# Kernel tuning notes

Measured on AMD Instinct MI355X. Metric: run time of the kernel, lower is better.

Reference implementation:

```python
import jax, jax.numpy as jnp
import numpy as np
import math

H = 12  # heads (init kwarg)
KEEP_RATE = 0.7  # forward arg keep_rate (< 1 -> token pruning path)


def setup_inputs() -> dict:
    key = jax.random.key(0)
    k0, k1, k2 = jax.random.split(key, 3)
    b, n, c = 32, 577, 768  # ViT-B/16 @ 384px: 576 patches + CLS
    x = jax.random.normal(k0, (b, n, c), dtype=jnp.float32)
    # nn.Linear(dim, dim*3) and nn.Linear(dim, dim); kaiming-ish scale
    W_qkv = jax.random.normal(k1, (c, 3 * c), dtype=jnp.float32) / np.sqrt(c).astype(np.float32)
    b_qkv = jnp.zeros((3 * c,), dtype=jnp.float32)
    W_out = jax.random.normal(k2, (c, c), dtype=jnp.float32) / np.sqrt(c).astype(np.float32)
    b_out = jnp.zeros((c,), dtype=jnp.float32)
    return {"x": x, "keep_rate": KEEP_RATE, "W_qkv": W_qkv, "b_qkv": b_qkv,
            "W_out": W_out, "b_out": b_out}


def reference(x, keep_rate, W_qkv, b_qkv, W_out, b_out):
    b, n, c = x.shape
    d = c // H
    scale = (c / H) ** -0.5
    # qkv projection + split into heads: 'b n (h d) -> b h n d'
    qkv = x @ W_qkv + b_qkv                      # [b, n, 3c]
    q, k, v = jnp.split(qkv, 3, axis=-1)
    split_heads = lambda t: t.reshape(b, n, H, d).transpose(0, 2, 1, 3)
    q, k, v = split_heads(q), split_heads(k), split_heads(v)
    dots = jnp.einsum('bhid,bhjd->bhij', q, k) * scale   # [b,h,n,n]
    attention = jax.nn.softmax(dots, axis=-1)
    out = jnp.einsum('bhij,bhjd->bhid', attention, v)    # [b,h,n,d]
    out = out.transpose(0, 2, 1, 3).reshape(b, n, c)     # 'b h n d -> b n (h d)'
    out = out @ W_out + b_out                            # to_out (dropout=0)
    final_tokens = n - 1
    if keep_rate < 1:
        final_tokens = math.ceil(keep_rate * final_tokens)
        # CLS-token attention to patch tokens, averaged over heads
        class_attention = attention[:, :, 0, 1:].mean(axis=1)   # [b, n-1]
        _, ind = jax.lax.top_k(class_attention, final_tokens)    # [b, final_tokens]
        ind = jnp.sort(ind, axis=1)
        index = jnp.broadcast_to(ind[:, :, None], (b, final_tokens, c))
        return (x, index, ind, class_attention, final_tokens)
    return (out, None, None, None, final_tokens)
```

## Files before the change

### kernel.cpp

```cpp
#include <hip/hip_runtime.h>
#include <math.h>

#define BATCH 32
#define NTOK 577
#define NPATCH 576
#define CDIM 768
#define HEADS 12
#define DHEAD 64
#define W3 2304
#define FT 404

#define WS_WTIL  24576
#define WS_DBIAS 319488
#define WS_DOTS  319872
#define WS_IND   541440

#define O_X      0ULL
#define O_INDEX  14180352ULL
#define O_IND    24109056ULL
#define O_CA     24121984ULL
#define O_FT     24140416ULL

#define NIDX4  2482176
#define NCOPY4 3545088

__global__ __launch_bounds__(512) void k_fold(const float* __restrict__ x,
                                              const float* __restrict__ W,
                                              const float* __restrict__ bq,
                                              float* __restrict__ wtil,
                                              float* __restrict__ dbias) {
    __shared__ float x0s[CDIM];
    __shared__ float red[512];
    __shared__ float qs[DHEAD];
    const int b = blockIdx.x, h = blockIdx.y, tid = threadIdx.x;
    if (tid < CDIM / 4)
        ((float4*)x0s)[tid] = ((const float4*)(x + (size_t)b * NTOK * CDIM))[tid];
    __syncthreads();
    {
        const int d = tid & 63, seg = tid >> 6;
        const float* Wq = W + h * DHEAD + d;
        const int c0 = seg * 96;
        float acc = 0.f;
        #pragma unroll 32
        for (int c = c0; c < c0 + 96; c++) acc += x0s[c] * Wq[(size_t)c * W3];
        red[tid] = acc;
    }
    __syncthreads();
    if (tid < DHEAD) {
        float q = red[tid];
        #pragma unroll
        for (int s = 1; s < 8; s++) q += red[tid + s * 64];
        q += bq[h * DHEAD + tid];
        qs[tid] = q;
        float t = q * bq[CDIM + h * DHEAD + tid];
        #pragma unroll
        for (int off = 32; off; off >>= 1) t += __shfl_down(t, off);
        if (tid == 0) dbias[b * HEADS + h] = t;
    }
    __syncthreads();
    for (int c = tid; c < CDIM; c += 512) {
        const float* wr = W + (size_t)c * W3 + CDIM + h * DHEAD;
        float acc = 0.f;
        #pragma unroll
        for (int d = 0; d < DHEAD; d += 4) {
            float4 a = *reinterpret_cast<const float4*>(wr + d);
            acc += a.x * qs[d] + a.y * qs[d + 1] + a.z * qs[d + 2] + a.w * qs[d + 3];
        }
        wtil[((size_t)b * HEADS + h) * CDIM + c] = acc;
    }
}

#define LOADG(A, G)                                                               \
    {                                                                             \
        _Pragma("unroll")                                                         \
        for (int u = 0; u < 4; u++) {                                             \
            const int j = jbase + (G) * 4 + u;                                    \
            if (j < NTOK) {                                                       \
                const float4* xp =                                                \
                    (const float4*)(x + ((size_t)b * NTOK + j) * CDIM);           \
                A[u][0] = xp[lane]; A[u][1] = xp[64 + lane]; A[u][2] = xp[128 + lane]; \
            } else {                                                              \
                A[u][0] = A[u][1] = A[u][2] = make_float4(0.f, 0.f, 0.f, 0.f);    \
            }                                                                     \
        }                                                                         \
    }

#define COMPG(A, G)                                                               \
    {                                                                             \
        float acc[4][3];                                                          \
        _Pragma("unroll")                                                         \
        for (int u = 0; u < 4; u++) { acc[u][0] = acc[u][1] = acc[u][2] = 0.f; }  \
        _Pragma("unroll")                                                         \
        for (int i = 0; i < 3; i++)                                               \
            _Pragma("unroll")                                                     \
            for (int u = 0; u < 4; u++)                                           \
                _Pragma("unroll")                                                 \
                for (int hh = 0; hh < 3; hh++)                                    \
                    acc[u][hh] += A[u][i].x * wr[hh][i].x + A[u][i].y * wr[hh][i].y \
                                + A[u][i].z * wr[hh][i].z + A[u][i].w * wr[hh][i].w; \
        _Pragma("unroll")                                                         \
        for (int off = 32; off; off >>= 1)                                        \
            _Pragma("unroll")                                                     \
            for (int u = 0; u < 4; u++)                                           \
                _Pragma("unroll")                                                 \
                for (int hh = 0; hh < 3; hh++)                                    \
                    acc[u][hh] += __shfl_xor(acc[u][hh], off);                    \
        if (lane == 0) {                                                          \
            _Pragma("unroll")                                                     \
            for (int u = 0; u < 4; u++) {                                         \
                const int j = jbase + (G) * 4 + u;                                \
                if (j < NTOK) {                                                   \
                    _Pragma("unroll")                                             \
                    for (int hh = 0; hh < 3; hh++)                                \
                        dots[((size_t)b * HEADS + h0 + hh) * NTOK + j] =          \
                            0.125f * (acc[u][hh] + db[hh]);                       \
                }                                                                 \
            }                                                                     \
        }                                                                         \
    }

__global__ __launch_bounds__(256, 3) void k_dots(const float* __restrict__ x,
                                                 const float* __restrict__ wtil,
                                                 const float* __restrict__ dbias,
                                                 float* __restrict__ dots) {
    const int b = blockIdx.x, tid = threadIdx.x;
    const int w = tid >> 6, lane = tid & 63, h0 = w * 3;
    float4 wr[3][3];
    float db[3];
    #pragma unroll
    for (int hh = 0; hh < 3; hh++) {
        #pragma unroll
        for (int i = 0; i < 3; i++)
            wr[hh][i] = *reinterpret_cast<const float4*>(
                wtil + ((size_t)b * HEADS + h0 + hh) * CDIM + i * 256 + lane * 4);
        db[hh] = dbias[b * HEADS + h0 + hh];
    }
    const int jbase = blockIdx.y * 16;
    float4 abuf[4][3], nbuf[4][3];
    LOADG(abuf, 0);
    LOADG(nbuf, 1);
    COMPG(abuf, 0);
    LOADG(abuf, 2);
    COMPG(nbuf, 1);
    LOADG(nbuf, 3);
    COMPG(abuf, 2);
    COMPG(nbuf, 3);
}

__global__ __launch_bounds__(512) void k_catopk(const float* __restrict__ dots,
                                                float* __restrict__ out,
                                                int* __restrict__ indws,
                                                int write_ft) {
    __shared__ float dl[HEADS * NTOK];
    __shared__ float mh[HEADS], sh[HEADS];
    __shared__ unsigned vals[NPATCH];
    __shared__ unsigned long long segmask[9];
    __shared__ int segoff[9];
    const int b = blockIdx.x, tid = threadIdx.x;
    {
        const float4* s4 = (const float4*)(dots + (size_t)b * HEADS * NTOK);
        float4* d4 = (float4*)dl;
        for (int i = tid; i < HEADS * NTOK / 4; i += 512) d4[i] = s4[i];
    }
    __syncthreads();
    const int w = tid >> 6, lane = tid & 63;
    for (int h = w; h < HEADS; h += 8) {
        const float* row = dl + h * NTOK;
        float m = -3.4e38f;
        for (int j = lane; j < NTOK; j += 64) m = fmaxf(m, row[j]);
        #pragma unroll
        for (int off = 32; off; off >>= 1) m = fmaxf(m, __shfl_xor(m, off));
        float s = 0.f;
        for (int j = lane; j < NTOK; j += 64) s += expf(row[j] - m);
        #pragma unroll
        for (int off = 32; off; off >>= 1) s += __shfl_xor(s, off);
        if (lane == 0) { mh[h] = m; sh[h] = s; }
    }
    __syncthreads();
    for (int t = tid; t < NPATCH; t += 512) {
        float ca = 0.f;
        #pragma unroll
        for (int h = 0; h < HEADS; h++)
            ca += expf(dl[h * NTOK + 1 + t] - mh[h]) / sh[h];
        ca *= (1.f / 12.f);
        out[O_CA + (size_t)b * NPATCH + t] = ca;
        vals[t] = __float_as_uint(ca);
    }
    __syncthreads();
    {
        const uint4* v4 = (const uint4*)vals;
        for (int s = w; s < 9; s += 8) {
            const int t = s * 64 + lane;
            const unsigned myv = vals[t];
            int rank = 0;
            #pragma unroll 8
            for (int j4 = 0; j4 < NPATCH / 4; j4++) {
                const uint4 vv = v4[j4];
                const int j = j4 * 4;
                rank += (vv.x > myv) || (vv.x == myv && j     < t);
                rank += (vv.y > myv) || (vv.y == myv && j + 1 < t);
                rank += (vv.z > myv) || (vv.z == myv && j + 2 < t);
                rank += (vv.w > myv) || (vv.w == myv && j + 3 < t);
            }
            const unsigned long long mask = __ballot(rank < FT);
            if (lane == 0) segmask[s] = mask;
        }
    }
    __syncthreads();
    if (tid == 0) {
        int acc = 0;
        #pragma unroll
        for (int s = 0; s < 9; s++) { segoff[s] = acc; acc += __popcll(segmask[s]); }
    }
    __syncthreads();
    for (int s = w; s < 9; s += 8) {
        const int t = s * 64 + lane;
        const unsigned long long mask = segmask[s];
        if ((mask >> lane) & 1ull) {
            const int pos = segoff[s] + __popcll(mask & ((1ull << lane) - 1ull));
            indws[b * FT + pos] = t;
            out[O_IND + (size_t)b * FT + pos] = (float)t;
        }
    }
    if (b == 0 && tid == 0 && write_ft) out[O_FT] = (float)FT;
}

__global__ __launch_bounds__(256) void k_bcast(const int* __restrict__ ind,
                                               const float* __restrict__ x,
                                               float* __restrict__ out) {
    const float4* x4 = (const float4*)x;
    float4* o4 = (float4*)(out + O_X);
    float4* i4 = (float4*)(out + O_INDEX);
    const unsigned stride = gridDim.x * 256u;
    for (unsigned g = blockIdx.x * 256u + threadIdx.x; g < NIDX4 + NCOPY4; g += stride) {
        if (g < NCOPY4) {
            o4[g] = x4[g];
        } else {
            const unsigned e = g - NCOPY4;
            const unsigned row = e / 192u;
            const float v = (float)ind[row];
            float4 o; o.x = v; o.y = v; o.z = v; o.w = v;
            i4[e] = o;
        }
    }
}

extern "C" void kernel_launch(void* const* d_in, const int* in_sizes, int n_in,
                              void* d_out, int out_size, void* d_ws, size_t ws_size,
                              hipStream_t stream) {
    const float* x  = (const float*)d_in[0];
    const float* W  = (const float*)d_in[2];
    const float* bq = (const float*)d_in[3];
    float* ws = (float*)d_ws;
    float* out = (float*)d_out;

    k_fold<<<dim3(BATCH, HEADS), 512, 0, stream>>>(x, W, bq, ws + WS_WTIL, ws + WS_DBIAS);
    k_dots<<<dim3(BATCH, 37), 256, 0, stream>>>(x, ws + WS_WTIL, ws + WS_DBIAS,
                                                ws + WS_DOTS);
    const int write_ft = (out_size > (int)O_FT) ? 1 : 0;
    k_catopk<<<BATCH, 512, 0, stream>>>(ws + WS_DOTS, out, (int*)(ws + WS_IND), write_ft);
    k_bcast<<<2048, 256, 0, stream>>>((const int*)(ws + WS_IND), x, out);
}
```

Measured before the change: 236.5 us.

## Tile k_dots over 64 tokens with shared-memory staging of x and folded weights

Rewrites the CLS-query dot kernel so each block handles 64 tokens for all 12 heads. The block stages the folded weights and 128-column chunks of x in LDS. Each thread accumulates a 4x12 register tile, and partial sums are reduced through shuffles and a shared buffer. This cuts the grid from 37 to 10 blocks per batch and removes the per-token full-wave shuffle reductions, at the cost of about 70KB of LDS per block, which lowers occupancy, and more __syncthreads barriers.

```diff
diff --git a/kernel.cpp b/kernel.cpp
--- a/kernel.cpp
+++ b/kernel.cpp
@@ -23,6 +23,8 @@
 
 #define NIDX4  2482176
 #define NCOPY4 3545088
+
+#define XROW 132
 
 __global__ __launch_bounds__(512) void k_fold(const float* __restrict__ x,
                                               const float* __restrict__ W,
@@ -70,81 +72,87 @@
     }
 }
 
-#define LOADG(A, G)                                                               \
-    {                                                                             \
-        _Pragma("unroll")                                                         \
-        for (int u = 0; u < 4; u++) {                                             \
-            const int j = jbase + (G) * 4 + u;                                    \
-            if (j < NTOK) {                                                       \
-                const float4* xp =                                                \
-                    (const float4*)(x + ((size_t)b * NTOK + j) * CDIM);           \
-                A[u][0] = xp[lane]; A[u][1] = xp[64 + lane]; A[u][2] = xp[128 + lane]; \
-            } else {                                                              \
-                A[u][0] = A[u][1] = A[u][2] = make_float4(0.f, 0.f, 0.f, 0.f);    \
-            }                                                                     \
-        }                                                                         \
-    }
-
-#define COMPG(A, G)                                                               \
-    {                                                                             \
-        float acc[4][3];                                                          \
-        _Pragma("unroll")                                                         \
-        for (int u = 0; u < 4; u++) { acc[u][0] = acc[u][1] = acc[u][2] = 0.f; }  \
-        _Pragma("unroll")                                                         \
-        for (int i = 0; i < 3; i++)                                               \
-            _Pragma("unroll")                                                     \
-            for (int u = 0; u < 4; u++)                                           \
-                _Pragma("unroll")                                                 \
-                for (int hh = 0; hh < 3; hh++)                                    \
-                    acc[u][hh] += A[u][i].x * wr[hh][i].x + A[u][i].y * wr[hh][i].y \
-                                + A[u][i].z * wr[hh][i].z + A[u][i].w * wr[hh][i].w; \
-        _Pragma("unroll")                                                         \
-        for (int off = 32; off; off >>= 1)                                        \
-            _Pragma("unroll")                                                     \
-            for (int u = 0; u < 4; u++)                                           \
-                _Pragma("unroll")                                                 \
-                for (int hh = 0; hh < 3; hh++)                                    \
-                    acc[u][hh] += __shfl_xor(acc[u][hh], off);                    \
-        if (lane == 0) {                                                          \
-            _Pragma("unroll")                                                     \
-            for (int u = 0; u < 4; u++) {                                         \
-                const int j = jbase + (G) * 4 + u;                                \
-                if (j < NTOK) {                                                   \
-                    _Pragma("unroll")                                             \
-                    for (int hh = 0; hh < 3; hh++)                                \
-                        dots[((size_t)b * HEADS + h0 + hh) * NTOK + j] =          \
-                            0.125f * (acc[u][hh] + db[hh]);                       \
-                }                                                                 \
-            }                                                                     \
-        }                                                                         \
-    }
-
-__global__ __launch_bounds__(256, 3) void k_dots(const float* __restrict__ x,
-                                                 const float* __restrict__ wtil,
-                                                 const float* __restrict__ dbias,
-                                                 float* __restrict__ dots) {
-    const int b = blockIdx.x, tid = threadIdx.x;
-    const int w = tid >> 6, lane = tid & 63, h0 = w * 3;
-    float4 wr[3][3];
-    float db[3];
+__global__ __launch_bounds__(256) void k_dots(const float* __restrict__ x,
+                                              const float* __restrict__ wtil,
+                                              const float* __restrict__ dbias,
+                                              float* __restrict__ dots) {
+    __shared__ __align__(16) float smem[64 * XROW + HEADS * CDIM];
+    float* const xt = smem;
+    float* const wt = smem + 64 * XROW;
+    float* const part = smem;
+    const int b = blockIdx.x, y = blockIdx.y, tid = threadIdx.x;
+    const int j0 = y * 64;
+    const int jq = tid & 15, cs = tid >> 4;
+    const int w = tid >> 6, lane = tid & 63;
+    {
+        const float4* s4 = (const float4*)(wtil + (size_t)b * HEADS * CDIM);
+        float4* d4 = (float4*)wt;
+        #pragma unroll
+        for (int i = 0; i < 9; i++) d4[tid + i * 256] = s4[tid + i * 256];
+    }
+    float acc[4][12];
     #pragma unroll
-    for (int hh = 0; hh < 3; hh++) {
-        #pragma unroll
-        for (int i = 0; i < 3; i++)
-            wr[hh][i] = *reinterpret_cast<const float4*>(
-                wtil + ((size_t)b * HEADS + h0 + hh) * CDIM + i * 256 + lane * 4);
-        db[hh] = dbias[b * HEADS + h0 + hh];
-    }
-    const int jbase = blockIdx.y * 16;
-    float4 abuf[4][3], nbuf[4][3];
-    LOADG(abuf, 0);
-    LOADG(nbuf, 1);
-    COMPG(abuf, 0);
-    LOADG(abuf, 2);
-    COMPG(nbuf, 1);
-    LOADG(nbuf, 3);
-    COMPG(abuf, 2);
-    COMPG(nbuf, 3);
+    for (int r = 0; r < 4; r++)
+        #pragma unroll
+        for (int h = 0; h < 12; h++) acc[r][h] = 0.f;
+    const float4* xg = (const float4*)x;
+    for (int k = 0; k < 6; k++) {
+        __syncthreads();
+        #pragma unroll
+        for (int i = 0; i < 8; i++) {
+            const int f = tid + i * 256;
+            const int row = f >> 5, col = f & 31;
+            float4 v = make_float4(0.f, 0.f, 0.f, 0.f);
+            if (j0 + row < NTOK)
+                v = xg[(size_t)(b * NTOK + j0 + row) * 192 + k * 32 + col];
+            *(float4*)&xt[row * XROW + col * 4] = v;
+        }
+        __syncthreads();
+        #pragma unroll
+        for (int f = 0; f < 2; f++) {
+            const int col4 = cs * 2 + f;
+            float4 xa[4];
+            #pragma unroll
+            for (int r = 0; r < 4; r++)
+                xa[r] = *(const float4*)&xt[(jq + 16 * r) * XROW + col4 * 4];
+            #pragma unroll
+            for (int h = 0; h < 12; h++) {
+                const float4 wv = *(const float4*)&wt[h * CDIM + k * 128 + col4 * 4];
+                #pragma unroll
+                for (int r = 0; r < 4; r++)
+                    acc[r][h] += xa[r].x * wv.x + xa[r].y * wv.y
+                               + xa[r].z * wv.z + xa[r].w * wv.w;
+            }
+        }
+    }
+    #pragma unroll
+    for (int off = 16; off <= 32; off <<= 1)
+        #pragma unroll
+        for (int r = 0; r < 4; r++)
+            #pragma unroll
+            for (int h = 0; h < 12; h++)
+                acc[r][h] += __shfl_xor(acc[r][h], off);
+    __syncthreads();
+    if (lane < 16) {
+        #pragma unroll
+        for (int r = 0; r < 4; r++)
+            #pragma unroll
+            for (int h = 0; h < 12; h++)
+                part[w * 768 + lane * 48 + r * 12 + h] = acc[r][h];
+    }
+    __syncthreads();
+    #pragma unroll
+    for (int s = 0; s < 3; s++) {
+        const int o = tid + s * 256;
+        const int jq2 = o / 48, rh = o - jq2 * 48;
+        const int r = rh / 12, h = rh - r * 12;
+        const int j = j0 + jq2 + 16 * r;
+        if (j < NTOK) {
+            const float sum = part[o] + part[768 + o] + part[1536 + o] + part[2304 + o];
+            dots[((size_t)b * HEADS + h) * NTOK + j] =
+                0.125f * (sum + dbias[b * HEADS + h]);
+        }
+    }
 }
 
 __global__ __launch_bounds__(512) void k_catopk(const float* __restrict__ dots,
@@ -255,7 +263,7 @@
     float* out = (float*)d_out;
 
     k_fold<<<dim3(BATCH, HEADS), 512, 0, stream>>>(x, W, bq, ws + WS_WTIL, ws + WS_DBIAS);
-    k_dots<<<dim3(BATCH, 37), 256, 0, stream>>>(x, ws + WS_WTIL, ws + WS_DBIAS,
+    k_dots<<<dim3(BATCH, 10), 256, 0, stream>>>(x, ws + WS_WTIL, ws + WS_DBIAS,
                                                 ws + WS_DOTS);
     const int write_ft = (out_size > (int)O_FT) ? 1 : 0;
     k_catopk<<<BATCH, 512, 0, stream>>>(ws + WS_DOTS, out, (int*)(ws + WS_IND), write_ft);
```

Result: slower. 251.9 us (+6.5%).
